# Kernel tuning notes

Hardware: AMD Instinct MI355X
Metric: run time of the kernel (lower is better)

The kernel has to match this reference:

```python
import jax, jax.numpy as jnp
import numpy as np

NUM_HEADS = 16
D_MODEL = 1024
HEAD_DIM = D_MODEL // NUM_HEADS
EMB = 1024
B, L = 2, 2048


def setup_inputs() -> dict:
    key = jax.random.key(0)
    k1, k2, k3 = jax.random.split(key, 3)
    scale_in = 1.0 / np.sqrt(EMB)
    scale_out = 1.0 / np.sqrt(D_MODEL)
    return {
        "x": jax.random.normal(k1, (B, L, EMB), dtype=jnp.float32),
        "W_qkv": jax.random.normal(k2, (EMB, 3 * D_MODEL), dtype=jnp.float32) * scale_in,
        "b_qkv": jnp.zeros((3 * D_MODEL,), dtype=jnp.float32),
        "W_out": jax.random.normal(k3, (D_MODEL, EMB), dtype=jnp.float32) * scale_out,
        "b_out": jnp.zeros((EMB,), dtype=jnp.float32),
    }


def reference(x, W_qkv, b_qkv, W_out, b_out):
    Bn, Ln, _ = x.shape
    qkv = x @ W_qkv + b_qkv  # [B, L, 3*d_model]
    q = qkv[:, :, :D_MODEL].reshape(Bn, Ln, NUM_HEADS, HEAD_DIM)
    k = qkv[:, :, D_MODEL:2 * D_MODEL].reshape(Bn, Ln, NUM_HEADS, HEAD_DIM)
    v = qkv[:, :, 2 * D_MODEL:].reshape(Bn, Ln, NUM_HEADS, HEAD_DIM)
    scores = jnp.einsum('bqhd,bkhd->bhqk', q, k)  # [B, H, L, L]
    attn = jax.nn.softmax(scores / jnp.sqrt(jnp.float32(HEAD_DIM)), axis=-1)
    out = jnp.einsum('bhqk,bkhd->bqhd', attn, v).reshape(Bn, Ln, D_MODEL)
    return out @ W_out + b_out
```

## Files before the change

### kernel.cpp

```cpp
#include <hip/hip_runtime.h>
#include <stdint.h>

#define B_   2
#define L_   2048
#define H_   16
#define D_   64
#define EMB_ 1024
#define DM_  1024
#define N3_  3072
#define TOK_ 4096

typedef unsigned short u16;
typedef unsigned int u32;
typedef __attribute__((ext_vector_type(4))) float f32x4;
typedef __attribute__((ext_vector_type(8))) short s16x8;
typedef __attribute__((ext_vector_type(4))) u32 u32x4;
typedef __attribute__((ext_vector_type(2))) u32 u32x2;
typedef __attribute__((ext_vector_type(4))) u16 u16x4;

#define MFMA(a,b,c) __builtin_amdgcn_mfma_f32_16x16x32_bf16(a,b,c,0,0,0)

#define AS1 __attribute__((address_space(1)))
#define AS3 __attribute__((address_space(3)))
#define GLLDS(g, l) __builtin_amdgcn_global_load_lds( \
    (const AS1 u32*)(const void*)(g), (AS3 u32*)(void*)(l), 16, 0, 0)

#define QSCALE 0.18033688011f

static __device__ __forceinline__ u16 f2bf(float f) {
  u32 u = __builtin_bit_cast(u32, f);
  return (u16)((u + 0x8000u) >> 16);
}

static __device__ __forceinline__ float bf2f(u16 v) {
  u32 u = ((u32)v) << 16;
  return __builtin_bit_cast(float, u);
}

static __device__ __forceinline__ u32 pack2bf(float a, float b) {
  u32 ua = __builtin_bit_cast(u32, a) + 0x8000u;
  u32 ub = __builtin_bit_cast(u32, b) + 0x8000u;
  return __builtin_amdgcn_perm(ub, ua, 0x07060302u);
}

static __device__ __forceinline__ float fexp2(float x) {
#if __has_builtin(__builtin_amdgcn_exp2f)
  return __builtin_amdgcn_exp2f(x);
#else
  float r;
  asm("v_exp_f32 %0, %1" : "=v"(r) : "v"(x));
  return r;
#endif
}

__global__ __launch_bounds__(256) void k_prep(
    const float* __restrict__ x,   u16* __restrict__ xb,
    const float* __restrict__ Wq,  u16* __restrict__ wqT,
    const float* __restrict__ Wo,  u16* __restrict__ woT)
{
  const int blk = blockIdx.x, tid = threadIdx.x;
  if (blk < 4096) {
    int i = (blk * 256 + tid) * 4;
    float4 v = *(const float4*)(x + i);
    ushort4 o;
    o.x = f2bf(v.x); o.y = f2bf(v.y); o.z = f2bf(v.z); o.w = f2bf(v.w);
    *(ushort4*)(xb + i) = o;
    return;
  }
  __shared__ float tile[32][33];
  const float* in;
  u16* out;
  int R, C, bx, by;
  if (blk < 4096 + 3072) {
    int t = blk - 4096;
    in = Wq; out = wqT; R = EMB_; C = N3_;
    bx = t % 96; by = t / 96;
  } else {
    int t = blk - 7168;
    in = Wo; out = woT; R = DM_; C = DM_;
    bx = t & 31; by = t >> 5;
  }
  int c0 = bx * 32, r0 = by * 32;
  int tx = tid & 31, ty = tid >> 5;
  #pragma unroll
  for (int i = 0; i < 32; i += 8)
    tile[ty + i][tx] = in[(size_t)(r0 + ty + i) * C + (c0 + tx)];
  __syncthreads();
  int c = tid >> 3, j = tid & 7;
  u16x4 o;
  #pragma unroll
  for (int r = 0; r < 4; ++r)
    o[r] = f2bf(tile[j * 4 + r][c]);
  *(u16x4*)(out + (size_t)(c0 + c) * R + r0 + j * 4) = o;
}

template<int EPI>
__global__ __launch_bounds__(256, 4) void k_gemm(
    const u16* __restrict__ A, const u16* __restrict__ Bt,
    const float* __restrict__ bias, int M, int N, int K,
    float* __restrict__ Cf,
    u16* __restrict__ Qo, u16* __restrict__ Ko, u16* __restrict__ Vo)
{
  const int tid = threadIdx.x;
  const int wave = tid >> 6, lane = tid & 63;
  const int lr = lane & 15, lk = lane >> 4;
  const int wr = wave >> 1, wc = wave & 1;
  const int m0 = blockIdx.y * 128, n0 = blockIdx.x * 128;

  __shared__ u16 As[2][128 * 32];
  __shared__ u16 Bs[2][128 * 32];

  f32x4 acc[4][4] = {};

  const int srow = wave * 32 + (lane >> 2);
  const int schunk = (lane & 3) * 8;
  const u16* gA = A  + (size_t)(m0 + srow) * K + schunk;
  const u16* gB = Bt + (size_t)(n0 + srow) * K + schunk;
  const size_t rstep = (size_t)16 * K;
  u16* lA0 = (u16*)As[0] + wave * (32 * 32);
  u16* lA1 = (u16*)As[1] + wave * (32 * 32);
  u16* lB0 = (u16*)Bs[0] + wave * (32 * 32);
  u16* lB1 = (u16*)Bs[1] + wave * (32 * 32);

  GLLDS(gA,         lA0);
  GLLDS(gA + rstep, lA0 + 16 * 32);
  GLLDS(gB,         lB0);
  GLLDS(gB + rstep, lB0 + 16 * 32);

  int buf = 0;
  for (int k0 = 0; k0 < K; k0 += 32, buf ^= 1) {
    __syncthreads();

    if (k0 + 32 < K) {
      u16* dA = buf ? lA0 : lA1;
      u16* dB = buf ? lB0 : lB1;
      GLLDS(gA + k0 + 32,         dA);
      GLLDS(gA + k0 + 32 + rstep, dA + 16 * 32);
      GLLDS(gB + k0 + 32,         dB);
      GLLDS(gB + k0 + 32 + rstep, dB + 16 * 32);
    }

    const u16* Ab = (const u16*)As[buf];
    const u16* Bb = (const u16*)Bs[buf];
    s16x8 af[4], bf[4];
    #pragma unroll
    for (int mi = 0; mi < 4; ++mi)
      af[mi] = *(const s16x8*)(Ab + (wr * 64 + mi * 16 + lr) * 32 + lk * 8);
    #pragma unroll
    for (int ni = 0; ni < 4; ++ni)
      bf[ni] = *(const s16x8*)(Bb + (wc * 64 + ni * 16 + lr) * 32 + lk * 8);
    #pragma unroll
    for (int mi = 0; mi < 4; ++mi)
      #pragma unroll
      for (int ni = 0; ni < 4; ++ni)
        acc[mi][ni] = MFMA(af[mi], bf[ni], acc[mi][ni]);
  }

  const int mbase = m0 + wr * 64 + lk * 4;
  #pragma unroll
  for (int ni = 0; ni < 4; ++ni) {
    int gn = n0 + wc * 64 + ni * 16 + lr;
    float bz = bias[gn];
    if (EPI == 1) {
      #pragma unroll
      for (int mi = 0; mi < 4; ++mi)
        #pragma unroll
        for (int r = 0; r < 4; ++r) {
          int gm = mbase + mi * 16 + r;
          Cf[(size_t)gm * N + gn] = acc[mi][ni][r] + bz;
        }
    } else {
      int sec = gn >> 10, cm = gn & 1023;
      int h = cm >> 6, d = cm & 63;
      if (sec == 2) {
        #pragma unroll
        for (int mi = 0; mi < 4; ++mi) {
          int gm0 = mbase + mi * 16;
          int b = gm0 >> 11, l0 = gm0 & 2047;
          int bh = b * H_ + h;
          u16x4 vv;
          #pragma unroll
          for (int r = 0; r < 4; ++r) vv[r] = f2bf(acc[mi][ni][r] + bz);
          *(u16x4*)(Vo + ((size_t)bh * D_ + d) * L_ + l0) = vv;
        }
      } else {
        #pragma unroll
        for (int mi = 0; mi < 4; ++mi)
          #pragma unroll
          for (int r = 0; r < 4; ++r) {
            int gm = mbase + mi * 16 + r;
            float v = acc[mi][ni][r] + bz;
            int b = gm >> 11, l = gm & 2047;
            int bh = b * H_ + h;
            if (sec == 0) Qo[((size_t)bh * L_ + l) * D_ + d] = f2bf(v * QSCALE);
            else          Ko[((size_t)bh * L_ + l) * D_ + d] = f2bf(v);
          }
      }
    }
  }
}

__global__ __launch_bounds__(256, 2) void k_flash(
    const u16* __restrict__ Q, const u16* __restrict__ Kb,
    const u16* __restrict__ Vt,
    u16* __restrict__ O0, u16* __restrict__ O1, float* __restrict__ lpart)
{
  const int tid = threadIdx.x;
  const int wave = tid >> 6, lane = tid & 63;
  const int lr = lane & 15, lk = lane >> 4;
  const int blk = blockIdx.x;
  const int idx = blk >> 3;
  const int bh = (blk & 7) * 4 + (idx >> 4);
  const int rem = idx & 15;
  const int qt = rem >> 1;
  const int half = rem & 1;
  const int tbase = half * 1024;
  const int b = bh >> 4, h = bh & 15;
  const u16* Qh = Q  + (size_t)bh * L_ * D_;
  const u16* Kh = Kb + (size_t)bh * L_ * D_;
  const u16* Vh = Vt + (size_t)bh * D_ * L_;

  __shared__ u16 Ks[2][64 * 64];
  __shared__ u16 Vs[2][64 * 64];
  __shared__ u16 Ps[256 * 64];

  const int qrow0 = qt * 256 + wave * 64;
  s16x8 qf[4][2];
  #pragma unroll
  for (int g = 0; g < 4; ++g)
    #pragma unroll
    for (int ks = 0; ks < 2; ++ks)
      qf[g][ks] = *(const s16x8*)(Qh + (size_t)(qrow0 + g * 16 + lr) * D_ + ks * 32 + lk * 8);

  f32x4 acco[4][4] = {};
  float lst[4] = {0.f, 0.f, 0.f, 0.f};

  const int srow0 = wave * 16 + (lane >> 3);
  const int gch8 = (((lane & 7) ^ ((lane >> 3) & 7)) * 8);
  u16* kd0 = (u16*)Ks[0] + wave * (16 * 64);
  u16* kd1 = (u16*)Ks[1] + wave * (16 * 64);
  u16* vd0 = (u16*)Vs[0] + wave * (16 * 64);
  u16* vd1 = (u16*)Vs[1] + wave * (16 * 64);

  const int ck0 = (lk ^ (lr & 7)) * 8;
  const int sxor = (lr & 7) << 1;
  u16* PsW = Ps + wave * (64 * 64);

  GLLDS(Kh + (size_t)(tbase + srow0) * 64 + gch8,       kd0);
  GLLDS(Kh + (size_t)(tbase + srow0 + 8) * 64 + gch8,   kd0 + 8 * 64);
  GLLDS(Vh + ((size_t)srow0 * L_ + tbase + gch8),       vd0);
  GLLDS(Vh + ((size_t)(srow0 + 8) * L_ + tbase + gch8), vd0 + 8 * 64);

  int buf = 0;
  for (int t0 = tbase; t0 < tbase + 1024; t0 += 64, buf ^= 1) {
    __syncthreads();

    if (t0 + 64 < tbase + 1024) {
      const int tn = t0 + 64;
      u16* kd = buf ? kd0 : kd1;
      u16* vd = buf ? vd0 : vd1;
      GLLDS(Kh + (size_t)(tn + srow0) * 64 + gch8,       kd);
      GLLDS(Kh + (size_t)(tn + srow0 + 8) * 64 + gch8,   kd + 8 * 64);
      GLLDS(Vh + ((size_t)srow0 * L_ + tn + gch8),       vd);
      GLLDS(Vh + ((size_t)(srow0 + 8) * L_ + tn + gch8), vd + 8 * 64);
    }

    const u16* Kbuf = (const u16*)Ks[buf];
    f32x4 accs[4][4] = {};
    s16x8 kf[4][2];
    #pragma unroll
    for (int mi = 0; mi < 4; ++mi) {
      const u16* rp = Kbuf + (mi * 16 + lr) * 64;
      kf[mi][0] = *(const s16x8*)(rp + ck0);
      kf[mi][1] = *(const s16x8*)(rp + (ck0 ^ 32));
    }
    #pragma unroll
    for (int mi = 0; mi < 4; ++mi)
      #pragma unroll
      for (int g = 0; g < 4; ++g) {
        accs[g][mi] = MFMA(kf[mi][0], qf[g][0], accs[g][mi]);
        accs[g][mi] = MFMA(kf[mi][1], qf[g][1], accs[g][mi]);
      }

    #pragma unroll
    for (int g = 0; g < 4; ++g) {
      const int prow = (g * 16 + lr) * 64;
      #pragma unroll
      for (int mi = 0; mi < 4; ++mi) {
        float p0 = fexp2(accs[g][mi][0]);
        float p1 = fexp2(accs[g][mi][1]);
        float p2 = fexp2(accs[g][mi][2]);
        float p3 = fexp2(accs[g][mi][3]);
        lst[g] += (p0 + p1) + (p2 + p3);
        u32x2 pk = { pack2bf(p0, p1), pack2bf(p2, p3) };
        *(u32x2*)(PsW + prow + (((4 * mi + lk) ^ sxor) * 4)) = pk;
      }
    }

    const u16* Vbuf = (const u16*)Vs[buf];
    s16x8 vf[4][2], pf[4][2];
    #pragma unroll
    for (int di = 0; di < 4; ++di) {
      const u16* rp = Vbuf + (di * 16 + lr) * 64;
      vf[di][0] = *(const s16x8*)(rp + ck0);
      vf[di][1] = *(const s16x8*)(rp + (ck0 ^ 32));
    }
    #pragma unroll
    for (int g = 0; g < 4; ++g) {
      const int prow = (g * 16 + lr) * 64;
      pf[g][0] = *(const s16x8*)(PsW + prow + (((2 * lk) ^ sxor) * 4));
      pf[g][1] = *(const s16x8*)(PsW + prow + (((8 + 2 * lk) ^ sxor) * 4));
    }
    #pragma unroll
    for (int di = 0; di < 4; ++di)
      #pragma unroll
      for (int g = 0; g < 4; ++g) {
        acco[g][di] = MFMA(vf[di][0], pf[g][0], acco[g][di]);
        acco[g][di] = MFMA(vf[di][1], pf[g][1], acco[g][di]);
      }
  }

  u16* Oh = half ? O1 : O0;
  #pragma unroll
  for (int g = 0; g < 4; ++g) {
    float l = lst[g];
    l += __shfl_xor(l, 16);
    l += __shfl_xor(l, 32);
    const int q = qrow0 + g * 16 + lr;
    if (lk == 0)
      lpart[((size_t)(half << 5) + bh) * L_ + q] = l;
    #pragma unroll
    for (int di = 0; di < 4; ++di) {
      u16x4 o;
      #pragma unroll
      for (int r = 0; r < 4; ++r)
        o[r] = f2bf(acco[g][di][r]);
      *(u16x4*)(Oh + (size_t)(b * L_ + q) * DM_ + h * D_ + di * 16 + lk * 4) = o;
    }
  }
}

__global__ __launch_bounds__(256) void k_comb(
    const u16* O0, const u16* O1, const float* lpart, u16* AO)
{
  const int row = blockIdx.x;
  const int b = row >> 11, l = row & 2047;
  const int c = threadIdx.x * 4;
  const int h = c >> 6;
  const size_t bhl = (size_t)(b * H_ + h) * L_ + l;
  const float rl = 1.0f / (lpart[bhl] + lpart[(size_t)32 * L_ + bhl]);
  const size_t off = (size_t)row * DM_ + c;
  u16x4 a = *(const u16x4*)(O0 + off);
  u16x4 bb = *(const u16x4*)(O1 + off);
  u16x4 o;
  #pragma unroll
  for (int r = 0; r < 4; ++r)
    o[r] = f2bf((bf2f(a[r]) + bf2f(bb[r])) * rl);
  *(u16x4*)(AO + off) = o;
}

extern "C" void kernel_launch(void* const* d_in, const int* in_sizes, int n_in,
                              void* d_out, int out_size, void* d_ws, size_t ws_size,
                              hipStream_t stream)
{
  const float* x    = (const float*)d_in[0];
  const float* Wqkv = (const float*)d_in[1];
  const float* bqkv = (const float*)d_in[2];
  const float* Wout = (const float*)d_in[3];
  const float* bout = (const float*)d_in[4];
  float* out = (float*)d_out;

  u16* xb  = (u16*)d_ws;
  u16* wqT = xb  + (size_t)TOK_ * EMB_;
  u16* woT = wqT + (size_t)N3_ * EMB_;
  u16* qb  = woT + (size_t)DM_ * EMB_;
  u16* kb  = qb  + (size_t)B_ * H_ * L_ * D_;
  u16* vt  = kb  + (size_t)B_ * H_ * L_ * D_;
  u16* ao  = vt  + (size_t)B_ * H_ * L_ * D_;
  float* lpart = (float*)wqT;

  k_prep<<<4096 + 3072 + 1024, 256, 0, stream>>>(x, xb, Wqkv, wqT, Wout, woT);
  k_gemm<0><<<dim3(N3_ / 128, TOK_ / 128), 256, 0, stream>>>(
      xb, wqT, bqkv, TOK_, N3_, EMB_, nullptr, qb, kb, vt);
  k_flash<<<512, 256, 0, stream>>>(qb, kb, vt, ao, xb, lpart);
  k_comb<<<TOK_, 256, 0, stream>>>(ao, xb, lpart, ao);
  k_gemm<1><<<dim3(DM_ / 128, TOK_ / 128), 256, 0, stream>>>(
      ao, woT, bout, TOK_, DM_, EMB_, out, nullptr, nullptr, nullptr);
}
```

Before: 188.0 us.

## Keep attention probabilities in registers, split keys four ways, narrow output GEMM tile

After: 281.0 us. +49.5%, slower.

```diff
diff --git a/kernel.cpp b/kernel.cpp
--- a/kernel.cpp
+++ b/kernel.cpp
@@ -14,11 +14,26 @@
 typedef unsigned int u32;
 typedef __attribute__((ext_vector_type(4))) float f32x4;
 typedef __attribute__((ext_vector_type(8))) short s16x8;
+typedef __attribute__((ext_vector_type(4))) short s16x4;
 typedef __attribute__((ext_vector_type(4))) u32 u32x4;
 typedef __attribute__((ext_vector_type(2))) u32 u32x2;
 typedef __attribute__((ext_vector_type(4))) u16 u16x4;
 
 #define MFMA(a,b,c) __builtin_amdgcn_mfma_f32_16x16x32_bf16(a,b,c,0,0,0)
+
+#if defined(__has_builtin)
+#if __has_builtin(__builtin_amdgcn_mfma_f32_16x16x16bf16_1k)
+#define MFMA16(a,b,c) __builtin_amdgcn_mfma_f32_16x16x16bf16_1k(a,b,c,0,0,0)
+#endif
+#endif
+#ifndef MFMA16
+static __device__ __forceinline__ f32x4 mfma16_asm(s16x4 a, s16x4 b, f32x4 c) {
+  asm volatile("v_mfma_f32_16x16x16_bf16 %0, %1, %2, %0"
+               : "+v"(c) : "v"(a), "v"(b));
+  return c;
+}
+#define MFMA16(a,b,c) mfma16_asm(a,b,c)
+#endif
 
 #define AS1 __attribute__((address_space(1)))
 #define AS3 __attribute__((address_space(3)))
@@ -35,6 +50,16 @@
 static __device__ __forceinline__ float bf2f(u16 v) {
   u32 u = ((u32)v) << 16;
   return __builtin_bit_cast(float, u);
+}
+
+static __device__ __forceinline__ u16 f2h(float f) {
+  _Float16 h = (_Float16)f;
+  return __builtin_bit_cast(u16, h);
+}
+
+static __device__ __forceinline__ float h2f(u16 v) {
+  _Float16 h = __builtin_bit_cast(_Float16, v);
+  return (float)h;
 }
 
 static __device__ __forceinline__ u32 pack2bf(float a, float b) {
@@ -94,38 +119,41 @@
   *(u16x4*)(out + (size_t)(c0 + c) * R + r0 + j * 4) = o;
 }
 
-template<int EPI>
+template<int EPI, int BN>
 __global__ __launch_bounds__(256, 4) void k_gemm(
     const u16* __restrict__ A, const u16* __restrict__ Bt,
     const float* __restrict__ bias, int M, int N, int K,
     float* __restrict__ Cf,
     u16* __restrict__ Qo, u16* __restrict__ Ko, u16* __restrict__ Vo)
 {
+  constexpr int NF = BN / 32;
+  constexpr int BROWS = (BN == 128) ? 32 : 16;
   const int tid = threadIdx.x;
   const int wave = tid >> 6, lane = tid & 63;
   const int lr = lane & 15, lk = lane >> 4;
   const int wr = wave >> 1, wc = wave & 1;
-  const int m0 = blockIdx.y * 128, n0 = blockIdx.x * 128;
+  const int m0 = blockIdx.y * 128, n0 = blockIdx.x * BN;
 
   __shared__ u16 As[2][128 * 32];
-  __shared__ u16 Bs[2][128 * 32];
-
-  f32x4 acc[4][4] = {};
+  __shared__ u16 Bs[2][BN * 32];
+
+  f32x4 acc[4][NF] = {};
 
   const int srow = wave * 32 + (lane >> 2);
+  const int srowB = (BN == 128) ? srow : (wave * 16 + (lane >> 2));
   const int schunk = (lane & 3) * 8;
   const u16* gA = A  + (size_t)(m0 + srow) * K + schunk;
-  const u16* gB = Bt + (size_t)(n0 + srow) * K + schunk;
+  const u16* gB = Bt + (size_t)(n0 + srowB) * K + schunk;
   const size_t rstep = (size_t)16 * K;
   u16* lA0 = (u16*)As[0] + wave * (32 * 32);
   u16* lA1 = (u16*)As[1] + wave * (32 * 32);
-  u16* lB0 = (u16*)Bs[0] + wave * (32 * 32);
-  u16* lB1 = (u16*)Bs[1] + wave * (32 * 32);
+  u16* lB0 = (u16*)Bs[0] + wave * (BROWS * 32);
+  u16* lB1 = (u16*)Bs[1] + wave * (BROWS * 32);
 
   GLLDS(gA,         lA0);
   GLLDS(gA + rstep, lA0 + 16 * 32);
   GLLDS(gB,         lB0);
-  GLLDS(gB + rstep, lB0 + 16 * 32);
+  if (BN == 128) GLLDS(gB + rstep, lB0 + 16 * 32);
 
   int buf = 0;
   for (int k0 = 0; k0 < K; k0 += 32, buf ^= 1) {
@@ -137,29 +165,29 @@
       GLLDS(gA + k0 + 32,         dA);
       GLLDS(gA + k0 + 32 + rstep, dA + 16 * 32);
       GLLDS(gB + k0 + 32,         dB);
-      GLLDS(gB + k0 + 32 + rstep, dB + 16 * 32);
+      if (BN == 128) GLLDS(gB + k0 + 32 + rstep, dB + 16 * 32);
     }
 
     const u16* Ab = (const u16*)As[buf];
     const u16* Bb = (const u16*)Bs[buf];
-    s16x8 af[4], bf[4];
+    s16x8 af[4], bfr[NF];
     #pragma unroll
     for (int mi = 0; mi < 4; ++mi)
       af[mi] = *(const s16x8*)(Ab + (wr * 64 + mi * 16 + lr) * 32 + lk * 8);
     #pragma unroll
-    for (int ni = 0; ni < 4; ++ni)
-      bf[ni] = *(const s16x8*)(Bb + (wc * 64 + ni * 16 + lr) * 32 + lk * 8);
+    for (int ni = 0; ni < NF; ++ni)
+      bfr[ni] = *(const s16x8*)(Bb + (wc * (BN / 2) + ni * 16 + lr) * 32 + lk * 8);
     #pragma unroll
     for (int mi = 0; mi < 4; ++mi)
       #pragma unroll
-      for (int ni = 0; ni < 4; ++ni)
-        acc[mi][ni] = MFMA(af[mi], bf[ni], acc[mi][ni]);
+      for (int ni = 0; ni < NF; ++ni)
+        acc[mi][ni] = MFMA(af[mi], bfr[ni], acc[mi][ni]);
   }
 
   const int mbase = m0 + wr * 64 + lk * 4;
   #pragma unroll
-  for (int ni = 0; ni < 4; ++ni) {
-    int gn = n0 + wc * 64 + ni * 16 + lr;
+  for (int ni = 0; ni < NF; ++ni) {
+    int gn = n0 + wc * (BN / 2) + ni * 16 + lr;
     float bz = bias[gn];
     if (EPI == 1) {
       #pragma unroll
@@ -200,21 +228,24 @@
   }
 }
 
-__global__ __launch_bounds__(256, 2) void k_flash(
+__global__ __launch_bounds__(256, 3) void k_flash(
     const u16* __restrict__ Q, const u16* __restrict__ Kb,
     const u16* __restrict__ Vt,
-    u16* __restrict__ O0, u16* __restrict__ O1, float* __restrict__ lpart)
+    u16* __restrict__ O0, u16* __restrict__ O1,
+    u16* __restrict__ O2, u16* __restrict__ O3,
+    float* __restrict__ lpart, int lg)
 {
   const int tid = threadIdx.x;
   const int wave = tid >> 6, lane = tid & 63;
   const int lr = lane & 15, lk = lane >> 4;
   const int blk = blockIdx.x;
   const int idx = blk >> 3;
-  const int bh = (blk & 7) * 4 + (idx >> 4);
-  const int rem = idx & 15;
-  const int qt = rem >> 1;
-  const int half = rem & 1;
-  const int tbase = half * 1024;
+  const int bh = (blk & 7) * 4 + (idx >> (3 + lg));
+  const int rem = idx & ((8 << lg) - 1);
+  const int qt = rem >> lg;
+  const int part = rem & ((1 << lg) - 1);
+  const int klen = L_ >> lg;
+  const int tbase = part * klen;
   const int b = bh >> 4, h = bh & 15;
   const u16* Qh = Q  + (size_t)bh * L_ * D_;
   const u16* Kh = Kb + (size_t)bh * L_ * D_;
@@ -222,7 +253,6 @@
 
   __shared__ u16 Ks[2][64 * 64];
   __shared__ u16 Vs[2][64 * 64];
-  __shared__ u16 Ps[256 * 64];
 
   const int qrow0 = qt * 256 + wave * 64;
   s16x8 qf[4][2];
@@ -234,6 +264,7 @@
 
   f32x4 acco[4][4] = {};
   float lst[4] = {0.f, 0.f, 0.f, 0.f};
+  const f32x4 zz = {0.f, 0.f, 0.f, 0.f};
 
   const int srow0 = wave * 16 + (lane >> 3);
   const int gch8 = (((lane & 7) ^ ((lane >> 3) & 7)) * 8);
@@ -242,9 +273,10 @@
   u16* vd0 = (u16*)Vs[0] + wave * (16 * 64);
   u16* vd1 = (u16*)Vs[1] + wave * (16 * 64);
 
-  const int ck0 = (lk ^ (lr & 7)) * 8;
-  const int sxor = (lr & 7) << 1;
-  u16* PsW = Ps + wave * (64 * 64);
+  const int sx7 = lr & 7;
+  const int ck0 = (lk ^ sx7) * 8;
+  const int vsub = (lk & 1) * 4;
+  const int vx = lk >> 1;
 
   GLLDS(Kh + (size_t)(tbase + srow0) * 64 + gch8,       kd0);
   GLLDS(Kh + (size_t)(tbase + srow0 + 8) * 64 + gch8,   kd0 + 8 * 64);
@@ -252,10 +284,11 @@
   GLLDS(Vh + ((size_t)(srow0 + 8) * L_ + tbase + gch8), vd0 + 8 * 64);
 
   int buf = 0;
-  for (int t0 = tbase; t0 < tbase + 1024; t0 += 64, buf ^= 1) {
+  const int tend = tbase + klen;
+  for (int t0 = tbase; t0 < tend; t0 += 64, buf ^= 1) {
     __syncthreads();
 
-    if (t0 + 64 < tbase + 1024) {
+    if (t0 + 64 < tend) {
       const int tn = t0 + 64;
       u16* kd = buf ? kd0 : kd1;
       u16* vd = buf ? vd0 : vd1;
@@ -266,61 +299,34 @@
     }
 
     const u16* Kbuf = (const u16*)Ks[buf];
-    f32x4 accs[4][4] = {};
-    s16x8 kf[4][2];
+    const u16* Vbuf = (const u16*)Vs[buf];
     #pragma unroll
     for (int mi = 0; mi < 4; ++mi) {
       const u16* rp = Kbuf + (mi * 16 + lr) * 64;
-      kf[mi][0] = *(const s16x8*)(rp + ck0);
-      kf[mi][1] = *(const s16x8*)(rp + (ck0 ^ 32));
-    }
-    #pragma unroll
-    for (int mi = 0; mi < 4; ++mi)
+      s16x8 kf0 = *(const s16x8*)(rp + ck0);
+      s16x8 kf1 = *(const s16x8*)(rp + (ck0 ^ 32));
+      const int vofs = ((2 * mi + vx) ^ sx7) * 8 + vsub;
+      s16x4 vf[4];
+      #pragma unroll
+      for (int di = 0; di < 4; ++di)
+        vf[di] = *(const s16x4*)(Vbuf + (di * 16 + lr) * 64 + vofs);
       #pragma unroll
       for (int g = 0; g < 4; ++g) {
-        accs[g][mi] = MFMA(kf[mi][0], qf[g][0], accs[g][mi]);
-        accs[g][mi] = MFMA(kf[mi][1], qf[g][1], accs[g][mi]);
-      }
-
-    #pragma unroll
-    for (int g = 0; g < 4; ++g) {
-      const int prow = (g * 16 + lr) * 64;
-      #pragma unroll
-      for (int mi = 0; mi < 4; ++mi) {
-        float p0 = fexp2(accs[g][mi][0]);
-        float p1 = fexp2(accs[g][mi][1]);
-        float p2 = fexp2(accs[g][mi][2]);
-        float p3 = fexp2(accs[g][mi][3]);
+        f32x4 s = MFMA(kf0, qf[g][0], zz);
+        s = MFMA(kf1, qf[g][1], s);
+        float p0 = fexp2(s[0]), p1 = fexp2(s[1]);
+        float p2 = fexp2(s[2]), p3 = fexp2(s[3]);
         lst[g] += (p0 + p1) + (p2 + p3);
-        u32x2 pk = { pack2bf(p0, p1), pack2bf(p2, p3) };
-        *(u32x2*)(PsW + prow + (((4 * mi + lk) ^ sxor) * 4)) = pk;
+        u32x2 pw = { pack2bf(p0, p1), pack2bf(p2, p3) };
+        s16x4 pk = __builtin_bit_cast(s16x4, pw);
+        #pragma unroll
+        for (int di = 0; di < 4; ++di)
+          acco[g][di] = MFMA16(vf[di], pk, acco[g][di]);
       }
     }
-
-    const u16* Vbuf = (const u16*)Vs[buf];
-    s16x8 vf[4][2], pf[4][2];
-    #pragma unroll
-    for (int di = 0; di < 4; ++di) {
-      const u16* rp = Vbuf + (di * 16 + lr) * 64;
-      vf[di][0] = *(const s16x8*)(rp + ck0);
-      vf[di][1] = *(const s16x8*)(rp + (ck0 ^ 32));
-    }
-    #pragma unroll
-    for (int g = 0; g < 4; ++g) {
-      const int prow = (g * 16 + lr) * 64;
-      pf[g][0] = *(const s16x8*)(PsW + prow + (((2 * lk) ^ sxor) * 4));
-      pf[g][1] = *(const s16x8*)(PsW + prow + (((8 + 2 * lk) ^ sxor) * 4));
-    }
-    #pragma unroll
-    for (int di = 0; di < 4; ++di)
-      #pragma unroll
-      for (int g = 0; g < 4; ++g) {
-        acco[g][di] = MFMA(vf[di][0], pf[g][0], acco[g][di]);
-        acco[g][di] = MFMA(vf[di][1], pf[g][1], acco[g][di]);
-      }
-  }
-
-  u16* Oh = half ? O1 : O0;
+  }
+
+  u16* Oh = (part == 0) ? O0 : (part == 1) ? O1 : (part == 2) ? O2 : O3;
   #pragma unroll
   for (int g = 0; g < 4; ++g) {
     float l = lst[g];
@@ -328,34 +334,50 @@
     l += __shfl_xor(l, 32);
     const int q = qrow0 + g * 16 + lr;
     if (lk == 0)
-      lpart[((size_t)(half << 5) + bh) * L_ + q] = l;
+      lpart[((size_t)(part << 5) + bh) * L_ + q] = l;
     #pragma unroll
     for (int di = 0; di < 4; ++di) {
       u16x4 o;
       #pragma unroll
       for (int r = 0; r < 4; ++r)
-        o[r] = f2bf(acco[g][di][r]);
+        o[r] = f2h(acco[g][di][r]);
       *(u16x4*)(Oh + (size_t)(b * L_ + q) * DM_ + h * D_ + di * 16 + lk * 4) = o;
     }
   }
 }
 
 __global__ __launch_bounds__(256) void k_comb(
-    const u16* O0, const u16* O1, const float* lpart, u16* AO)
+    const u16* __restrict__ O0, const u16* __restrict__ O1,
+    const u16* __restrict__ O2, const u16* __restrict__ O3,
+    const float* __restrict__ lpart, u16* __restrict__ AO, int nsplit)
 {
   const int row = blockIdx.x;
   const int b = row >> 11, l = row & 2047;
   const int c = threadIdx.x * 4;
   const int h = c >> 6;
   const size_t bhl = (size_t)(b * H_ + h) * L_ + l;
-  const float rl = 1.0f / (lpart[bhl] + lpart[(size_t)32 * L_ + bhl]);
+  float ls = lpart[bhl] + lpart[(size_t)32 * L_ + bhl];
+  if (nsplit == 4)
+    ls += lpart[(size_t)64 * L_ + bhl] + lpart[(size_t)96 * L_ + bhl];
+  const float rl = 1.0f / ls;
   const size_t off = (size_t)row * DM_ + c;
   u16x4 a = *(const u16x4*)(O0 + off);
   u16x4 bb = *(const u16x4*)(O1 + off);
+  float s[4];
+  #pragma unroll
+  for (int r = 0; r < 4; ++r)
+    s[r] = h2f(a[r]) + h2f(bb[r]);
+  if (nsplit == 4) {
+    u16x4 cc = *(const u16x4*)(O2 + off);
+    u16x4 dd = *(const u16x4*)(O3 + off);
+    #pragma unroll
+    for (int r = 0; r < 4; ++r)
+      s[r] += h2f(cc[r]) + h2f(dd[r]);
+  }
   u16x4 o;
   #pragma unroll
   for (int r = 0; r < 4; ++r)
-    o[r] = f2bf((bf2f(a[r]) + bf2f(bb[r])) * rl);
+    o[r] = f2bf(s[r] * rl);
   *(u16x4*)(AO + off) = o;
 }
 
@@ -377,13 +399,19 @@
   u16* kb  = qb  + (size_t)B_ * H_ * L_ * D_;
   u16* vt  = kb  + (size_t)B_ * H_ * L_ * D_;
   u16* ao  = vt  + (size_t)B_ * H_ * L_ * D_;
+  u16* o2  = ao  + (size_t)TOK_ * DM_;
+  u16* o3  = o2  + (size_t)TOK_ * DM_;
   float* lpart = (float*)wqT;
 
+  const size_t need4 = (size_t)((const char*)(o3 + (size_t)TOK_ * DM_) - (const char*)d_ws);
+  const int lg = (ws_size >= need4) ? 2 : 1;
+  const int nsplit = 1 << lg;
+
   k_prep<<<4096 + 3072 + 1024, 256, 0, stream>>>(x, xb, Wqkv, wqT, Wout, woT);
-  k_gemm<0><<<dim3(N3_ / 128, TOK_ / 128), 256, 0, stream>>>(
+  k_gemm<0, 128><<<dim3(N3_ / 128, TOK_ / 128), 256, 0, stream>>>(
       xb, wqT, bqkv, TOK_, N3_, EMB_, nullptr, qb, kb, vt);
-  k_flash<<<512, 256, 0, stream>>>(qb, kb, vt, ao, xb, lpart);
-  k_comb<<<TOK_, 256, 0, stream>>>(ao, xb, lpart, ao);
-  k_gemm<1><<<dim3(DM_ / 128, TOK_ / 128), 256, 0, stream>>>(
+  k_flash<<<256 * nsplit, 256, 0, stream>>>(qb, kb, vt, ao, xb, o2, o3, lpart, lg);
+  k_comb<<<TOK_, 256, 0, stream>>>(ao, xb, o2, o3, lpart, ao, nsplit);
+  k_gemm<1, 64><<<dim3(DM_ / 64, TOK_ / 128), 256, 0, stream>>>(
       ao, woT, bout, TOK_, DM_, EMB_, out, nullptr, nullptr, nullptr);
 }
```
